# Kernel tuning notes

Hardware: AMD Instinct MI355X
Metric: run time of the kernel (lower is better)

The kernel has to match this reference:

```python
import jax, jax.numpy as jnp
import numpy as np

B, T, C = 2, 2048, 1024
H, HS = 16, 64          # num_heads, head_size; H*HS == C
FF = 4 * C
EPS = 1e-5


def setup_inputs() -> dict:
    key = jax.random.key(0)
    ks = jax.random.split(key, 10)
    s = 0.02
    return {
        "x": jax.random.normal(ks[0], (B, T, C), dtype=jnp.float32),
        "Wq": jax.random.normal(ks[1], (H, C, HS), dtype=jnp.float32) * s,
        "Wk": jax.random.normal(ks[2], (H, C, HS), dtype=jnp.float32) * s,
        "Wv": jax.random.normal(ks[3], (H, C, HS), dtype=jnp.float32) * s,
        "p": jnp.ones((H,), dtype=jnp.float32),  # per-head learnable scale, init 1
        "Wproj": jax.random.normal(ks[4], (C, C), dtype=jnp.float32) * s,
        "W1": jax.random.normal(ks[5], (C, FF), dtype=jnp.float32) * s,
        "W2": jax.random.normal(ks[6], (FF, C), dtype=jnp.float32) * s,
        "ln1_w": jnp.ones((C,), dtype=jnp.float32),
        "ln1_b": jnp.zeros((C,), dtype=jnp.float32),
        "ln2_w": jnp.ones((C,), dtype=jnp.float32),
        "ln2_b": jnp.zeros((C,), dtype=jnp.float32),
    }


def _layernorm(x, w, b):
    mu = jnp.mean(x, axis=-1, keepdims=True)
    var = jnp.mean(jnp.square(x - mu), axis=-1, keepdims=True)
    return (x - mu) * jax.lax.rsqrt(var + EPS) * w + b


def reference(x, Wq, Wk, Wv, p, Wproj, W1, W2, ln1_w, ln1_b, ln2_w, ln2_b):
    # --- multi-head causal self-attention (dropout p=0 -> identity) ---
    h = _layernorm(x, ln1_w, ln1_b)
    q = jnp.einsum("btc,hcs->bhts", h, Wq)  # [B,H,T,HS]
    k = jnp.einsum("btc,hcs->bhts", h, Wk)
    v = jnp.einsum("btc,hcs->bhts", h, Wv)
    scale = p ** (-0.5)  # per-head scale, p init to 1
    wei = jnp.einsum("bhts,bhks->bhtk", q, k) * scale[None, :, None, None]
    causal = jnp.tril(jnp.ones((T, T), dtype=bool))
    wei = jnp.where(causal[None, None], wei, -jnp.inf)
    wei = jax.nn.softmax(wei, axis=-1)
    att = jnp.einsum("bhtk,bhks->bhts", wei, v)          # [B,H,T,HS]
    att = att.transpose(0, 2, 1, 3).reshape(B, T, C)     # concat heads
    sa = att @ Wproj
    x = x + sa
    # --- feed-forward (activation_id=0 -> ReLU) ---
    h2 = _layernorm(x, ln2_w, ln2_b)
    ff = jax.nn.relu(h2 @ W1) @ W2
    return x + ff
```

## Files before the change

### kernel.cpp

```cpp
#include <hip/hip_runtime.h>


typedef _Float16 f16;
typedef _Float16 f16x8 __attribute__((ext_vector_type(8)));
typedef _Float16 f16x4v __attribute__((ext_vector_type(4)));
typedef float f32x4 __attribute__((ext_vector_type(4)));

static constexpr int Tn = 2048;
static constexpr int Cn = 1024;
static constexpr int HSn = 64;

__device__ __forceinline__ void glds16(const f16* g, f16* l) {
    __builtin_amdgcn_global_load_lds((const __attribute__((address_space(1))) void*)g,
                                     (__attribute__((address_space(3))) void*)l,
                                     16, 0, 0);
}

#define VMCNT(N) asm volatile("s_waitcnt vmcnt(" #N ")" ::: "memory")
__device__ __forceinline__ void barrier_raw() {
    asm volatile("" ::: "memory");
    __builtin_amdgcn_s_barrier();
    asm volatile("" ::: "memory");
}

__global__ __launch_bounds__(256) void ln_kernel(const float* __restrict__ x,
                                                 const float* __restrict__ w,
                                                 const float* __restrict__ b,
                                                 f16* __restrict__ out) {
    int row = blockIdx.x;
    const float* xr = x + (size_t)row * Cn;
    int tid = threadIdx.x, l = tid & 63, wv = tid >> 6;
    float4 v = *(const float4*)(xr + tid * 4);
    float s = v.x + v.y + v.z + v.w;
    float sq = v.x * v.x + v.y * v.y + v.z * v.z + v.w * v.w;
#pragma unroll
    for (int off = 32; off > 0; off >>= 1) {
        s += __shfl_down(s, off);
        sq += __shfl_down(sq, off);
    }
    __shared__ float red[8];
    if (l == 0) { red[wv] = s; red[wv + 4] = sq; }
    __syncthreads();
    float ts = red[0] + red[1] + red[2] + red[3];
    float tq = red[4] + red[5] + red[6] + red[7];
    float mean = ts * (1.0f / Cn);
    float var = tq * (1.0f / Cn) - mean * mean;
    float rstd = rsqrtf(var + 1e-5f);
    float4 wv4 = *(const float4*)(w + tid * 4);
    float4 bv4 = *(const float4*)(b + tid * 4);
    f16x4v o;
    o[0] = (f16)((v.x - mean) * rstd * wv4.x + bv4.x);
    o[1] = (f16)((v.y - mean) * rstd * wv4.y + bv4.y);
    o[2] = (f16)((v.z - mean) * rstd * wv4.z + bv4.z);
    o[3] = (f16)((v.w - mean) * rstd * wv4.w + bv4.w);
    *(f16x4v*)(out + (size_t)row * Cn + tid * 4) = o;
}

__global__ __launch_bounds__(256) void tr_cast_f32(const float* __restrict__ in, int irs,
                                                   f16* __restrict__ out, int ors) {
    __shared__ float tile[32][33];
    int r0 = blockIdx.x * 32, c0 = blockIdx.y * 32;
    int t = threadIdx.x;
    int rr = t >> 3, c4 = (t & 7) * 4;
    float4 v = *(const float4*)(in + (size_t)(r0 + rr) * irs + c0 + c4);
    tile[rr][c4] = v.x; tile[rr][c4 + 1] = v.y; tile[rr][c4 + 2] = v.z; tile[rr][c4 + 3] = v.w;
    __syncthreads();
    int cc = t >> 3, r4 = (t & 7) * 4;
    f16x4v o;
    o[0] = (f16)tile[r4][cc];
    o[1] = (f16)tile[r4 + 1][cc];
    o[2] = (f16)tile[r4 + 2][cc];
    o[3] = (f16)tile[r4 + 3][cc];
    *(f16x4v*)(out + (size_t)(c0 + cc) * ors + r0 + r4) = o;
}

__global__ __launch_bounds__(256) void tr_cast_qkv(const float* __restrict__ Wq,
                                                   const float* __restrict__ Wk,
                                                   const float* __restrict__ Wv,
                                                   f16* __restrict__ out) {
    int z = blockIdx.z;
    int qkv = z >> 4, h = z & 15;
    const float* in = (qkv == 0 ? Wq : qkv == 1 ? Wk : Wv) + (size_t)h * Cn * HSn;
    f16* o = out + (size_t)(qkv * Cn + h * HSn) * Cn;
    __shared__ float tile[32][33];
    int r0 = blockIdx.x * 32, c0 = blockIdx.y * 32;
    int t = threadIdx.x;
    int rr = t >> 3, c4 = (t & 7) * 4;
    float4 v = *(const float4*)(in + (size_t)(r0 + rr) * HSn + c0 + c4);
    tile[rr][c4] = v.x; tile[rr][c4 + 1] = v.y; tile[rr][c4 + 2] = v.z; tile[rr][c4 + 3] = v.w;
    __syncthreads();
    int cc = t >> 3, r4 = (t & 7) * 4;
    f16x4v ov;
    ov[0] = (f16)tile[r4][cc];
    ov[1] = (f16)tile[r4 + 1][cc];
    ov[2] = (f16)tile[r4 + 2][cc];
    ov[3] = (f16)tile[r4 + 3][cc];
    *(f16x4v*)(o + (size_t)(c0 + cc) * Cn + r0 + r4) = ov;
}

__global__ __launch_bounds__(256) void tr_vT(const f16* __restrict__ QKV, f16* __restrict__ vT) {
    int bh = blockIdx.z;
    int b = bh >> 4, h = bh & 15;
    const f16* in = QKV + (size_t)b * Tn * 3072 + 2048 + h * HSn;
    f16* out = vT + (size_t)bh * HSn * Tn;
    int r0 = blockIdx.x * 64;
    __shared__ __align__(16) f16 tile[64][72];
    int t = threadIdx.x;
#pragma unroll
    for (int i = 0; i < 2; i++) {
        int f = i * 256 + t;
        int rr = f >> 3, c8 = (f & 7) * 8;
        *(uint4*)(&tile[rr][c8]) = *(const uint4*)(in + (size_t)(r0 + rr) * 3072 + c8);
    }
    __syncthreads();
#pragma unroll
    for (int i = 0; i < 2; i++) {
        int f = i * 256 + t;
        int cc = f >> 3, r8 = (f & 7) * 8;
        union { f16 h[8]; uint4 v; } u;
#pragma unroll
        for (int j = 0; j < 8; j++) u.h[j] = tile[r8 + j][cc];
        *(uint4*)(out + (size_t)cc * Tn + r0 + r8) = u.v;
    }
}

template <int EPI>
__global__ __launch_bounds__(512, 2) void gemm8(const f16* __restrict__ A, const f16* __restrict__ Bt,
                                                f16* __restrict__ Cout, int M, int N, int K) {
    __shared__ __align__(16) f16 Abuf[4][8192];
    __shared__ __align__(16) f16 Bbuf[4][8192];
    int wg = blockIdx.x;
    int xcd = wg & 7, idx = wg >> 3;
    int bm = xcd * 2 + (idx & 1), bn = idx >> 1;
    int tid = threadIdx.x, l = tid & 63, w = tid >> 6;
    int wr = w >> 2, wc = w & 3;

    f32x4 acc[8][4];
#pragma unroll
    for (int m = 0; m < 8; m++)
#pragma unroll
        for (int n = 0; n < 4; n++) acc[m][n] = f32x4{0.f, 0.f, 0.f, 0.f};

    int l15 = l & 15;
    int lane_off = l15 * 32 + (((l >> 4) ^ ((l15 >> 1) & 3)) << 3);
    const f16* Afr = &Abuf[0][wr * 4096 + lane_off];
    const f16* Bfr = &Bbuf[0][(wc >> 1) * 4096 + (wc & 1) * 2048 + lane_off];

    int srow = w * 16 + (l >> 2);
    int schunk = (l & 3) ^ ((l >> 3) & 3);
    const f16* agp = A + (size_t)(bm * 256 + srow) * K + schunk * 8;
    const f16* bgp = Bt + (size_t)(bn * 256 + srow) * K + schunk * 8;
    const size_t rK = (size_t)128 * K;
    f16* dstA = &Abuf[0][w * 512];
    f16* dstB = &Bbuf[0][w * 512];

    auto stage = [&](int kt, int bf) {
        int k0 = kt * 32;
        glds16(agp + k0, dstA + bf * 8192);
        glds16(agp + rK + k0, dstA + bf * 8192 + 4096);
        glds16(bgp + k0, dstB + bf * 8192);
        glds16(bgp + rK + k0, dstB + bf * 8192 + 4096);
    };

    int NT = K >> 5;
    stage(0, 0);
    stage(1, 1);
    stage(2, 2);
    for (int t = 0; t < NT; ++t) {
        int cb = t & 3;
        VMCNT(8);
        barrier_raw();
        const f16* Ab = Afr + cb * 8192;
        const f16* Bb = Bfr + cb * 8192;
        f16x8 af[4], bf4[4];
#pragma unroll
        for (int m = 0; m < 4; m++) af[m] = *(const f16x8*)(Ab + m * 512);
#pragma unroll
        for (int n = 0; n < 4; n++) bf4[n] = *(const f16x8*)(Bb + n * 512);
        if (t + 3 < NT) stage(t + 3, (t + 3) & 3);
        __builtin_amdgcn_s_setprio(1);
#pragma unroll
        for (int m = 0; m < 4; m++)
#pragma unroll
            for (int n = 0; n < 4; n++)
                acc[m][n] = __builtin_amdgcn_mfma_f32_16x16x32_f16(af[m], bf4[n], acc[m][n], 0, 0, 0);
        __builtin_amdgcn_s_setprio(0);
        barrier_raw();
#pragma unroll
        for (int m = 0; m < 4; m++) af[m] = *(const f16x8*)(Ab + (m + 4) * 512);
        __builtin_amdgcn_s_setprio(1);
#pragma unroll
        for (int m = 0; m < 4; m++)
#pragma unroll
            for (int n = 0; n < 4; n++)
                acc[m + 4][n] = __builtin_amdgcn_mfma_f32_16x16x32_f16(af[m], bf4[n], acc[m + 4][n], 0, 0, 0);
        __builtin_amdgcn_s_setprio(0);
    }
    VMCNT(0);

    int row0 = bm * 256 + wr * 128 + (l >> 4) * 4;
    int col0 = bn * 256 + wc * 64 + (l & 15);
#pragma unroll
    for (int m = 0; m < 8; m++) {
#pragma unroll
        for (int n = 0; n < 4; n++) {
#pragma unroll
            for (int r = 0; r < 4; r++) {
                size_t idx = (size_t)(row0 + m * 16 + r) * N + (col0 + n * 16);
                float v = acc[m][n][r];
                if constexpr (EPI == 1) v = fmaxf(v, 0.f);
                Cout[idx] = (f16)v;
            }
        }
    }
}

__device__ __forceinline__ void l2_map(int& bm, int& bn) {
    int wg = blockIdx.y * 32 + blockIdx.x;
    int x = wg & 7, idx = wg >> 3;
    bm = x * 4 + (idx & 3);
    bn = idx >> 2;
}

template <int EPI>
__global__ __launch_bounds__(512) void gemm_ks(const f16* __restrict__ A, const f16* __restrict__ Bt,
                                               void* __restrict__ Cout, const float* __restrict__ resid,
                                               int M, int N, int K) {
    __shared__ __align__(16) char smem[98304];
    f16* As = (f16*)smem;
    f16* Bs = (f16*)(smem + 49152);
    int bm, bn;
    l2_map(bm, bn);
    int tid = threadIdx.x, l = tid & 63, w = tid >> 6;
    int grp = w >> 2, wl = w & 3;
    int wr = wl >> 1, wc = wl & 1;
    int Kh = K >> 1;
    int KT = Kh >> 5;

    f32x4 acc[4][4];
#pragma unroll
    for (int m = 0; m < 4; m++)
#pragma unroll
        for (int n = 0; n < 4; n++) acc[m][n] = f32x4{0.f, 0.f, 0.f, 0.f};

    int schunk = (l & 3) ^ ((l >> 3) & 3);
    const f16* agp = A + (size_t)(bm * 128 + wl * 16 + (l >> 2)) * K + grp * Kh + schunk * 8;
    const f16* bgp = Bt + (size_t)(bn * 128 + wl * 16 + (l >> 2)) * K + grp * Kh + schunk * 8;
    const size_t half = (size_t)64 * K;
    f16* Ab = As + grp * 12288;
    f16* Bb = Bs + grp * 12288;

    auto stage = [&](int kt, int bf) {
        size_t k0 = (size_t)kt * 32;
        glds16(agp + k0, Ab + bf * 4096 + wl * 512);
        glds16(agp + half + k0, Ab + bf * 4096 + 2048 + wl * 512);
        glds16(bgp + k0, Bb + bf * 4096 + wl * 512);
        glds16(bgp + half + k0, Bb + bf * 4096 + 2048 + wl * 512);
    };

    int l15 = l & 15;
    int rbase = (wr * 64 + l15) * 32 + (((l >> 4) ^ ((l15 >> 1) & 3)) << 3);
    int cbase = (wc * 64 + l15) * 32 + (((l >> 4) ^ ((l15 >> 1) & 3)) << 3);

    stage(0, 0);
    if (KT > 1) stage(1, 1);
    int nb = 2;
    for (int kt = 0; kt < KT; ++kt) {
        int cb = kt % 3;
        if (kt + 1 < KT) VMCNT(4);
        else VMCNT(0);
        barrier_raw();
        if (kt + 2 < KT) { stage(kt + 2, nb); nb = (nb == 2) ? 0 : nb + 1; }
        f16x8 af[4], bfr[4];
#pragma unroll
        for (int m = 0; m < 4; m++) af[m] = *(const f16x8*)(Ab + cb * 4096 + rbase + m * 512);
#pragma unroll
        for (int n = 0; n < 4; n++) bfr[n] = *(const f16x8*)(Bb + cb * 4096 + cbase + n * 512);
        __builtin_amdgcn_s_setprio(1);
#pragma unroll
        for (int m = 0; m < 4; m++)
#pragma unroll
            for (int n = 0; n < 4; n++)
                acc[m][n] = __builtin_amdgcn_mfma_f32_16x16x32_f16(af[m], bfr[n], acc[m][n], 0, 0, 0);
        __builtin_amdgcn_s_setprio(0);
    }
    __syncthreads();

    float* red = (float*)smem;
#pragma unroll
    for (int m = 0; m < 4; m++) {
        if (grp == 1) {
#pragma unroll
            for (int n = 0; n < 4; n++)
                *(f32x4*)(red + wl * 1280 + l * 20 + n * 4) = acc[m][n];
        }
        __syncthreads();
        if (grp == 0) {
#pragma unroll
            for (int n = 0; n < 4; n++)
                acc[m][n] += *(const f32x4*)(red + wl * 1280 + l * 20 + n * 4);
        }
        __syncthreads();
    }

    if (grp == 0) {
        int row0 = bm * 128 + wr * 64 + (l >> 4) * 4;
        int col0 = bn * 128 + wc * 64 + (l & 15);
#pragma unroll
        for (int m = 0; m < 4; m++) {
#pragma unroll
            for (int n = 0; n < 4; n++) {
#pragma unroll
                for (int r = 0; r < 4; r++) {
                    size_t idx = (size_t)(row0 + m * 16 + r) * N + (col0 + n * 16);
                    float v = acc[m][n][r];
                    if constexpr (EPI == 0) ((f16*)Cout)[idx] = (f16)v;
                    else if constexpr (EPI == 1) ((f16*)Cout)[idx] = (f16)fmaxf(v, 0.f);
                    else ((float*)Cout)[idx] = v + resid[idx];
                }
            }
        }
    }
}

__global__ __launch_bounds__(256) void attn_kernel(const f16* __restrict__ QKV,
                                                   const f16* __restrict__ vT,
                                                   const float* __restrict__ p,
                                                   f16* __restrict__ att) {
    int wg = blockIdx.x;
    int x = wg & 7, idx = wg >> 3;
    int bh = x * 4 + (idx & 3);
    int pq = idx >> 2;
    int b = bh >> 4, h = bh & 15;
    int tid = threadIdx.x, w = tid >> 6, l = tid & 63;
    float sc2 = rsqrtf(p[h]) * 1.44269504f;

    __shared__ __align__(16) f16 Ks[2][4096];
    __shared__ __align__(16) f16 Vs[2][4096];
    __shared__ __align__(16) f16 Ps[4][16 * 80];
    f16* Pw = &Ps[w][0];

    int srow0 = tid >> 3;
    int c0 = (tid & 7) ^ (srow0 & 7);
    int srow1 = 32 + srow0;
    int c1 = (tid & 7) ^ (srow1 & 7);
    const f16* Kg = QKV + (size_t)b * Tn * 3072 + 1024 + h * HSn;
    const f16* Vg = vT + (size_t)bh * HSn * Tn;

    auto stageKV = [&](int kv0, int bf) {
        glds16(Kg + (size_t)(kv0 + srow0) * 3072 + c0 * 8, &Ks[bf][w * 512]);
        glds16(Kg + (size_t)(kv0 + srow1) * 3072 + c1 * 8, &Ks[bf][2048 + w * 512]);
        glds16(Vg + (size_t)srow0 * Tn + kv0 + c0 * 8, &Vs[bf][w * 512]);
        glds16(Vg + (size_t)srow1 * Tn + kv0 + c1 * 8, &Vs[bf][2048 + w * 512]);
    };

    for (int pass = 0; pass < 2; ++pass) {
        int qt = pass ? (31 - pq) : pq;
        int qg = qt * 64 + w * 16 + (l & 15);
        int qo = qt * 64 + w * 16 + (l >> 4) * 4;
        const f16* qptr = QKV + (size_t)(b * Tn + qg) * 3072 + h * HSn + (l >> 4) * 8;
        f16x8 qf0 = *(const f16x8*)(qptr);
        f16x8 qf1 = *(const f16x8*)(qptr + 32);
        f16 sch = (f16)sc2;
#pragma unroll
        for (int j = 0; j < 8; j++) { qf0[j] *= sch; qf1[j] *= sch; }

        f32x4 o[4];
#pragma unroll
        for (int nf = 0; nf < 4; nf++) o[nf] = f32x4{0.f, 0.f, 0.f, 0.f};
        float m_r = -1e30f, l_r = 0.f;

        int nt = qt + 1;
        stageKV(0, 0);
        __syncthreads();
        for (int t = 0; t < nt; ++t) {
            int cb = t & 1, kv0 = t * 64;
            if (t + 1 < nt) stageKV(kv0 + 64, cb ^ 1);
            const char* Kb = (const char*)&Ks[cb][0];
            const char* Vb = (const char*)&Vs[cb][0];
            f32x4 s[4];
#pragma unroll
            for (int n = 0; n < 4; n++) s[n] = f32x4{0.f, 0.f, 0.f, 0.f};
            __builtin_amdgcn_s_setprio(1);
#pragma unroll
            for (int n = 0; n < 4; n++) {
#pragma unroll
                for (int ks = 0; ks < 2; ks++) {
                    int boff = (n * 16 + (l & 15)) * 128 + (((ks * 32 + (l >> 4) * 8) * 2) ^ ((l & 7) << 4));
                    f16x8 kf = *(const f16x8*)(Kb + boff);
                    s[n] = __builtin_amdgcn_mfma_f32_16x16x32_f16(kf, ks == 0 ? qf0 : qf1, s[n], 0, 0, 0);
                }
            }
            __builtin_amdgcn_s_setprio(0);
            if (t == qt) {
                int rel = qg - kv0;
#pragma unroll
                for (int n = 0; n < 4; n++)
#pragma unroll
                    for (int r = 0; r < 4; r++) {
                        int kvr = n * 16 + (l >> 4) * 4 + r;
                        if (kvr > rel) s[n][r] = -1e30f;
                    }
            }
            float tmax = -1e30f;
#pragma unroll
            for (int n = 0; n < 4; n++)
#pragma unroll
                for (int r = 0; r < 4; r++) tmax = fmaxf(tmax, s[n][r]);
            tmax = fmaxf(tmax, __shfl_xor(tmax, 16));
            tmax = fmaxf(tmax, __shfl_xor(tmax, 32));
            float lmul = 1.f;
            if (__any(tmax > m_r + 8.f)) {
                float mnew = fmaxf(m_r, tmax);
                lmul = exp2f(m_r - mnew);
                m_r = mnew;
                float ar[4];
#pragma unroll
                for (int r = 0; r < 4; r++) ar[r] = __shfl(lmul, (l >> 4) * 4 + r);
#pragma unroll
                for (int nf = 0; nf < 4; nf++)
#pragma unroll
                    for (int r = 0; r < 4; r++) o[nf][r] *= ar[r];
            }
            float rsum = 0.f;
#pragma unroll
            for (int n = 0; n < 4; n++) {
                f16x4v pk;
#pragma unroll
                for (int r = 0; r < 4; r++) {
                    float e = exp2f(s[n][r] - m_r);
                    rsum += e;
                    pk[r] = (f16)e;
                }
                *(f16x4v*)(&Pw[(l & 15) * 80 + n * 16 + (l >> 4) * 4]) = pk;
            }
            rsum += __shfl_xor(rsum, 16);
            rsum += __shfl_xor(rsum, 32);
            l_r = l_r * lmul + rsum;
            f16x8 pa0 = *(const f16x8*)(&Pw[(l & 15) * 80 + (l >> 4) * 8]);
            f16x8 pa1 = *(const f16x8*)(&Pw[(l & 15) * 80 + 32 + (l >> 4) * 8]);
            __builtin_amdgcn_s_setprio(1);
#pragma unroll
            for (int nf = 0; nf < 4; nf++) {
#pragma unroll
                for (int ks = 0; ks < 2; ks++) {
                    int boff = (nf * 16 + (l & 15)) * 128 + (((ks * 32 + (l >> 4) * 8) * 2) ^ ((l & 7) << 4));
                    f16x8 vf = *(const f16x8*)(Vb + boff);
                    o[nf] = __builtin_amdgcn_mfma_f32_16x16x32_f16(ks == 0 ? pa0 : pa1, vf, o[nf], 0, 0, 0);
                }
            }
            __builtin_amdgcn_s_setprio(0);
            __syncthreads();
        }
        float lro[4];
#pragma unroll
        for (int r = 0; r < 4; r++) lro[r] = __shfl(l_r, (l >> 4) * 4 + r);
#pragma unroll
        for (int nf = 0; nf < 4; nf++) {
#pragma unroll
            for (int r = 0; r < 4; r++) {
                float v = o[nf][r] / lro[r];
                att[(size_t)(b * Tn + qo + r) * Cn + h * HSn + nf * 16 + (l & 15)] = (f16)v;
            }
        }
    }
}

extern "C" void kernel_launch(void* const* d_in, const int* in_sizes, int n_in,
                              void* d_out, int out_size, void* d_ws, size_t ws_size,
                              hipStream_t stream) {
    const float* x = (const float*)d_in[0];
    const float* Wq = (const float*)d_in[1];
    const float* Wk = (const float*)d_in[2];
    const float* Wv = (const float*)d_in[3];
    const float* p = (const float*)d_in[4];
    const float* Wproj = (const float*)d_in[5];
    const float* W1 = (const float*)d_in[6];
    const float* W2 = (const float*)d_in[7];
    const float* ln1w = (const float*)d_in[8];
    const float* ln1b = (const float*)d_in[9];
    const float* ln2w = (const float*)d_in[10];
    const float* ln2b = (const float*)d_in[11];

    char* ws = (char*)d_ws;
    const size_t MB = 1ull << 20;
    f16* Wqkv_t = (f16*)(ws + 0 * MB);
    f16* Wproj_t = (f16*)(ws + 6 * MB);
    f16* W1_t = (f16*)(ws + 8 * MB);
    f16* W2_t = (f16*)(ws + 16 * MB);
    float* x1 = (float*)(ws + 24 * MB);
    f16* QKV = (f16*)(ws + 40 * MB);
    f16* h1 = (f16*)(ws + 64 * MB);
    f16* vTb = (f16*)(ws + 64 * MB);
    f16* attb = (f16*)(ws + 72 * MB);
    f16* h2 = attb;
    f16* ffh = QKV;
    float* out = (float*)d_out;

    tr_cast_qkv<<<dim3(32, 2, 48), 256, 0, stream>>>(Wq, Wk, Wv, Wqkv_t);
    tr_cast_f32<<<dim3(32, 32), 256, 0, stream>>>(Wproj, 1024, Wproj_t, 1024);
    tr_cast_f32<<<dim3(32, 128), 256, 0, stream>>>(W1, 4096, W1_t, 1024);
    tr_cast_f32<<<dim3(128, 32), 256, 0, stream>>>(W2, 1024, W2_t, 4096);

    ln_kernel<<<4096, 256, 0, stream>>>(x, ln1w, ln1b, h1);
    gemm8<0><<<192, 512, 0, stream>>>(h1, Wqkv_t, QKV, 4096, 3072, 1024);
    tr_vT<<<dim3(32, 1, 32), 256, 0, stream>>>(QKV, vTb);
    attn_kernel<<<512, 256, 0, stream>>>(QKV, vTb, p, attb);
    gemm_ks<2><<<dim3(32, 8), 512, 0, stream>>>(attb, Wproj_t, x1, x, 4096, 1024, 1024);
    ln_kernel<<<4096, 256, 0, stream>>>(x1, ln2w, ln2b, h2);
    gemm8<1><<<256, 512, 0, stream>>>(h2, W1_t, ffh, 4096, 4096, 1024);
    gemm_ks<2><<<dim3(32, 8), 512, 0, stream>>>(ffh, W2_t, out, x1, 4096, 1024, 4096);
}
```

Before: 228.3 us.

## Launch one attention block per query tile, longest tiles first

Each attention workgroup previously handled a pair of query tiles (pq and 31-pq) so per-block causal work was balanced. Now it handles a single tile, with twice as many workgroups launched and tiles ordered from longest to shortest so the hardware scheduler can balance load dynamically. The per-iteration row-sum cross-lane shuffles are deferred to one reduction at the end, LDS fragment offsets are precomputed, and P is packed with cvt_pkrtz. The trade-off is more block launches and Q/prologue overhead per block, in exchange for more parallelism and less shuffle work in the inner loop.

```diff
diff --git a/kernel.cpp b/kernel.cpp
--- a/kernel.cpp
+++ b/kernel.cpp
@@ -21,6 +21,13 @@
     asm volatile("" ::: "memory");
     __builtin_amdgcn_s_barrier();
     asm volatile("" ::: "memory");
+}
+
+__device__ __forceinline__ unsigned cvt_pk_u32(float a, float b) {
+    auto v = __builtin_amdgcn_cvt_pkrtz(a, b);
+    union { __fp16 h2 __attribute__((ext_vector_type(2))); unsigned u; } c;
+    c.h2 = v;
+    return c.u;
 }
 
 __global__ __launch_bounds__(256) void ln_kernel(const float* __restrict__ x,
@@ -327,10 +334,9 @@
                                                    const f16* __restrict__ vT,
                                                    const float* __restrict__ p,
                                                    f16* __restrict__ att) {
-    int wg = blockIdx.x;
-    int x = wg & 7, idx = wg >> 3;
-    int bh = x * 4 + (idx & 3);
-    int pq = idx >> 2;
+    int i = blockIdx.x;
+    int bh = (i & 7) * 4 + ((i >> 3) & 3);
+    int qt = 31 - (i >> 5);
     int b = bh >> 4, h = bh & 15;
     int tid = threadIdx.x, w = tid >> 6, l = tid & 63;
     float sc2 = rsqrtf(p[h]) * 1.44269504f;
@@ -354,114 +360,115 @@
         glds16(Vg + (size_t)srow1 * Tn + kv0 + c1 * 8, &Vs[bf][2048 + w * 512]);
     };
 
-    for (int pass = 0; pass < 2; ++pass) {
-        int qt = pass ? (31 - pq) : pq;
-        int qg = qt * 64 + w * 16 + (l & 15);
-        int qo = qt * 64 + w * 16 + (l >> 4) * 4;
-        const f16* qptr = QKV + (size_t)(b * Tn + qg) * 3072 + h * HSn + (l >> 4) * 8;
-        f16x8 qf0 = *(const f16x8*)(qptr);
-        f16x8 qf1 = *(const f16x8*)(qptr + 32);
-        f16 sch = (f16)sc2;
-#pragma unroll
-        for (int j = 0; j < 8; j++) { qf0[j] *= sch; qf1[j] *= sch; }
-
-        f32x4 o[4];
-#pragma unroll
-        for (int nf = 0; nf < 4; nf++) o[nf] = f32x4{0.f, 0.f, 0.f, 0.f};
-        float m_r = -1e30f, l_r = 0.f;
-
-        int nt = qt + 1;
-        stageKV(0, 0);
+    int foff[8];
+#pragma unroll
+    for (int n = 0; n < 4; n++)
+#pragma unroll
+        for (int ks = 0; ks < 2; ks++)
+            foff[n * 2 + ks] = (n * 16 + (l & 15)) * 128 +
+                               (((ks * 32 + (l >> 4) * 8) * 2) ^ ((l & 7) << 4));
+
+    int qg = qt * 64 + w * 16 + (l & 15);
+    int qo = qt * 64 + w * 16 + (l >> 4) * 4;
+    const f16* qptr = QKV + (size_t)(b * Tn + qg) * 3072 + h * HSn + (l >> 4) * 8;
+    f16x8 qf0 = *(const f16x8*)(qptr);
+    f16x8 qf1 = *(const f16x8*)(qptr + 32);
+    f16 sch = (f16)sc2;
+#pragma unroll
+    for (int j = 0; j < 8; j++) { qf0[j] *= sch; qf1[j] *= sch; }
+
+    f32x4 o[4];
+#pragma unroll
+    for (int nf = 0; nf < 4; nf++) o[nf] = f32x4{0.f, 0.f, 0.f, 0.f};
+    float m_r = -1e30f, l_r = 0.f;
+
+    int nt = qt + 1;
+    stageKV(0, 0);
+    __syncthreads();
+    for (int t = 0; t < nt; ++t) {
+        int cb = t & 1, kv0 = t * 64;
+        if (t + 1 < nt) stageKV(kv0 + 64, cb ^ 1);
+        const char* Kb = (const char*)&Ks[cb][0];
+        const char* Vb = (const char*)&Vs[cb][0];
+        f32x4 s[4];
+#pragma unroll
+        for (int n = 0; n < 4; n++) s[n] = f32x4{0.f, 0.f, 0.f, 0.f};
+        __builtin_amdgcn_s_setprio(1);
+#pragma unroll
+        for (int n = 0; n < 4; n++)
+#pragma unroll
+            for (int ks = 0; ks < 2; ks++) {
+                f16x8 kf = *(const f16x8*)(Kb + foff[n * 2 + ks]);
+                s[n] = __builtin_amdgcn_mfma_f32_16x16x32_f16(kf, ks == 0 ? qf0 : qf1, s[n], 0, 0, 0);
+            }
+        __builtin_amdgcn_s_setprio(0);
+        if (t == qt) {
+            int rel = qg - kv0;
+#pragma unroll
+            for (int n = 0; n < 4; n++)
+#pragma unroll
+                for (int r = 0; r < 4; r++) {
+                    int kvr = n * 16 + (l >> 4) * 4 + r;
+                    if (kvr > rel) s[n][r] = -1e30f;
+                }
+        }
+        float tmax = -1e30f;
+#pragma unroll
+        for (int n = 0; n < 4; n++)
+#pragma unroll
+            for (int r = 0; r < 4; r++) tmax = fmaxf(tmax, s[n][r]);
+        tmax = fmaxf(tmax, __shfl_xor(tmax, 16));
+        tmax = fmaxf(tmax, __shfl_xor(tmax, 32));
+        float lmul = 1.f;
+        if (__any(tmax > m_r + 8.f)) {
+            float mnew = fmaxf(m_r, tmax);
+            lmul = exp2f(m_r - mnew);
+            m_r = mnew;
+            float ar[4];
+#pragma unroll
+            for (int r = 0; r < 4; r++) ar[r] = __shfl(lmul, (l >> 4) * 4 + r);
+#pragma unroll
+            for (int nf = 0; nf < 4; nf++)
+#pragma unroll
+                for (int r = 0; r < 4; r++) o[nf][r] *= ar[r];
+        }
+        float rsum = 0.f;
+#pragma unroll
+        for (int n = 0; n < 4; n++) {
+            float e0 = exp2f(s[n][0] - m_r), e1 = exp2f(s[n][1] - m_r);
+            float e2 = exp2f(s[n][2] - m_r), e3 = exp2f(s[n][3] - m_r);
+            rsum += (e0 + e1) + (e2 + e3);
+            union { unsigned u[2]; f16x4v h4; } u;
+            u.u[0] = cvt_pk_u32(e0, e1);
+            u.u[1] = cvt_pk_u32(e2, e3);
+            *(f16x4v*)(&Pw[(l & 15) * 80 + n * 16 + (l >> 4) * 4]) = u.h4;
+        }
+        l_r = l_r * lmul + rsum;
+        f16x8 pa0 = *(const f16x8*)(&Pw[(l & 15) * 80 + (l >> 4) * 8]);
+        f16x8 pa1 = *(const f16x8*)(&Pw[(l & 15) * 80 + 32 + (l >> 4) * 8]);
+        __builtin_amdgcn_s_setprio(1);
+#pragma unroll
+        for (int nf = 0; nf < 4; nf++)
+#pragma unroll
+            for (int ks = 0; ks < 2; ks++) {
+                f16x8 vf = *(const f16x8*)(Vb + foff[nf * 2 + ks]);
+                o[nf] = __builtin_amdgcn_mfma_f32_16x16x32_f16(ks == 0 ? pa0 : pa1, vf, o[nf], 0, 0, 0);
+            }
+        __builtin_amdgcn_s_setprio(0);
         __syncthreads();
-        for (int t = 0; t < nt; ++t) {
-            int cb = t & 1, kv0 = t * 64;
-            if (t + 1 < nt) stageKV(kv0 + 64, cb ^ 1);
-            const char* Kb = (const char*)&Ks[cb][0];
-            const char* Vb = (const char*)&Vs[cb][0];
-            f32x4 s[4];
-#pragma unroll
-            for (int n = 0; n < 4; n++) s[n] = f32x4{0.f, 0.f, 0.f, 0.f};
-            __builtin_amdgcn_s_setprio(1);
-#pragma unroll
-            for (int n = 0; n < 4; n++) {
-#pragma unroll
-                for (int ks = 0; ks < 2; ks++) {
-                    int boff = (n * 16 + (l & 15)) * 128 + (((ks * 32 + (l >> 4) * 8) * 2) ^ ((l & 7) << 4));
-                    f16x8 kf = *(const f16x8*)(Kb + boff);
-                    s[n] = __builtin_amdgcn_mfma_f32_16x16x32_f16(kf, ks == 0 ? qf0 : qf1, s[n], 0, 0, 0);
-                }
-            }
-            __builtin_amdgcn_s_setprio(0);
-            if (t == qt) {
-                int rel = qg - kv0;
-#pragma unroll
-                for (int n = 0; n < 4; n++)
-#pragma unroll
-                    for (int r = 0; r < 4; r++) {
-                        int kvr = n * 16 + (l >> 4) * 4 + r;
-                        if (kvr > rel) s[n][r] = -1e30f;
-                    }
-            }
-            float tmax = -1e30f;
-#pragma unroll
-            for (int n = 0; n < 4; n++)
-#pragma unroll
-                for (int r = 0; r < 4; r++) tmax = fmaxf(tmax, s[n][r]);
-            tmax = fmaxf(tmax, __shfl_xor(tmax, 16));
-            tmax = fmaxf(tmax, __shfl_xor(tmax, 32));
-            float lmul = 1.f;
-            if (__any(tmax > m_r + 8.f)) {
-                float mnew = fmaxf(m_r, tmax);
-                lmul = exp2f(m_r - mnew);
-                m_r = mnew;
-                float ar[4];
-#pragma unroll
-                for (int r = 0; r < 4; r++) ar[r] = __shfl(lmul, (l >> 4) * 4 + r);
-#pragma unroll
-                for (int nf = 0; nf < 4; nf++)
-#pragma unroll
-                    for (int r = 0; r < 4; r++) o[nf][r] *= ar[r];
-            }
-            float rsum = 0.f;
-#pragma unroll
-            for (int n = 0; n < 4; n++) {
-                f16x4v pk;
-#pragma unroll
-                for (int r = 0; r < 4; r++) {
-                    float e = exp2f(s[n][r] - m_r);
-                    rsum += e;
-                    pk[r] = (f16)e;
-                }
-                *(f16x4v*)(&Pw[(l & 15) * 80 + n * 16 + (l >> 4) * 4]) = pk;
-            }
-            rsum += __shfl_xor(rsum, 16);
-            rsum += __shfl_xor(rsum, 32);
-            l_r = l_r * lmul + rsum;
-            f16x8 pa0 = *(const f16x8*)(&Pw[(l & 15) * 80 + (l >> 4) * 8]);
-            f16x8 pa1 = *(const f16x8*)(&Pw[(l & 15) * 80 + 32 + (l >> 4) * 8]);
-            __builtin_amdgcn_s_setprio(1);
-#pragma unroll
-            for (int nf = 0; nf < 4; nf++) {
-#pragma unroll
-                for (int ks = 0; ks < 2; ks++) {
-                    int boff = (nf * 16 + (l & 15)) * 128 + (((ks * 32 + (l >> 4) * 8) * 2) ^ ((l & 7) << 4));
-                    f16x8 vf = *(const f16x8*)(Vb + boff);
-                    o[nf] = __builtin_amdgcn_mfma_f32_16x16x32_f16(ks == 0 ? pa0 : pa1, vf, o[nf], 0, 0, 0);
-                }
-            }
-            __builtin_amdgcn_s_setprio(0);
-            __syncthreads();
-        }
-        float lro[4];
-#pragma unroll
-        for (int r = 0; r < 4; r++) lro[r] = __shfl(l_r, (l >> 4) * 4 + r);
-#pragma unroll
-        for (int nf = 0; nf < 4; nf++) {
-#pragma unroll
-            for (int r = 0; r < 4; r++) {
-                float v = o[nf][r] / lro[r];
-                att[(size_t)(b * Tn + qo + r) * Cn + h * HSn + nf * 16 + (l & 15)] = (f16)v;
-            }
+    }
+    float lsum = l_r;
+    lsum += __shfl_xor(lsum, 16);
+    lsum += __shfl_xor(lsum, 32);
+    float lro[4];
+#pragma unroll
+    for (int r = 0; r < 4; r++) lro[r] = __shfl(lsum, (l >> 4) * 4 + r);
+#pragma unroll
+    for (int nf = 0; nf < 4; nf++) {
+#pragma unroll
+        for (int r = 0; r < 4; r++) {
+            float v = o[nf][r] / lro[r];
+            att[(size_t)(b * Tn + qo + r) * Cn + h * HSn + nf * 16 + (l & 15)] = (f16)v;
         }
     }
 }
@@ -505,7 +512,7 @@
     ln_kernel<<<4096, 256, 0, stream>>>(x, ln1w, ln1b, h1);
     gemm8<0><<<192, 512, 0, stream>>>(h1, Wqkv_t, QKV, 4096, 3072, 1024);
     tr_vT<<<dim3(32, 1, 32), 256, 0, stream>>>(QKV, vTb);
-    attn_kernel<<<512, 256, 0, stream>>>(QKV, vTb, p, attb);
+    attn_kernel<<<1024, 256, 0, stream>>>(QKV, vTb, p, attb);
     gemm_ks<2><<<dim3(32, 8), 512, 0, stream>>>(attb, Wproj_t, x1, x, 4096, 1024, 1024);
     ln_kernel<<<4096, 256, 0, stream>>>(x1, ln2w, ln2b, h2);
     gemm8<1><<<256, 512, 0, stream>>>(h2, W1_t, ffh, 4096, 4096, 1024);
```

Result: faster. 221.7 us (-2.9%).
